# Performance work log

Hardware: AMD Instinct MI355X
Metric: run time of the kernel (lower is better)

## Reference

```python
import jax, jax.numpy as jnp
import numpy as np

HEADS = 8
DIM_HEAD = 64
SCALE = DIM_HEAD ** -0.5


def entmax15(z, axis=-1):
    """Exact 1.5-entmax via the sort-based algorithm (Peters & Martins 2019)."""
    z = z / 2.0
    z = z - jnp.max(z, axis=axis, keepdims=True)  # shift-invariant, for stability
    zs = -jnp.sort(-z, axis=axis)  # descending
    n = z.shape[axis]
    k = jnp.arange(1, n + 1, dtype=z.dtype)
    mean = jnp.cumsum(zs, axis=axis) / k
    mean_sq = jnp.cumsum(zs * zs, axis=axis) / k
    ss = k * (mean_sq - mean * mean)
    delta = (1.0 - ss) / k
    tau = mean - jnp.sqrt(jnp.maximum(delta, 0.0))
    support = (tau <= zs).astype(jnp.int32)
    k_star = jnp.sum(support, axis=axis, keepdims=True)  # support size >= 1
    tau_star = jnp.take_along_axis(tau, k_star - 1, axis=axis)
    return jnp.square(jnp.maximum(z - tau_star, 0.0))


def setup_inputs() -> dict:
    key = jax.random.key(0)
    k1, k2, k3 = jax.random.split(key, 3)
    b, n, dim = 4, 1024, 512
    inner = HEADS * DIM_HEAD  # 512
    x = jax.random.normal(k1, (b, n, dim), dtype=jnp.float32)
    w_qkv = jax.random.normal(k2, (dim, inner * 3), dtype=jnp.float32) * 0.02
    w_out = jax.random.normal(k3, (inner, dim), dtype=jnp.float32) * 0.02
    return {"x": x, "w_qkv": w_qkv, "w_out": w_out}


def reference(x, w_qkv, w_out):
    b, n, dim = x.shape
    h, d = HEADS, DIM_HEAD
    qkv = x @ w_qkv  # [b, n, 3*h*d]
    q, k, v = jnp.split(qkv, 3, axis=-1)
    # [b, n, h*d] -> [b, h, n, d]
    def to_heads(t):
        return t.reshape(b, n, h, d).transpose(0, 2, 1, 3)
    q, k, v = to_heads(q) * SCALE, to_heads(k), to_heads(v)
    sim = jnp.einsum('bhid,bhjd->bhij', q, k)  # [b, h, n, n]
    attn = entmax15(sim, axis=-1)
    out = jnp.einsum('bhij,bhjd->bhid', attn, v)  # [b, h, n, d]
    out = out.transpose(0, 2, 1, 3).reshape(b, n, h * d)
    return out @ w_out
```

## Files before the change

### kernel.cpp

```cpp
#include <hip/hip_runtime.h>
#include <stdint.h>
#include <stddef.h>


typedef __attribute__((ext_vector_type(4))) float f32x4;
typedef __attribute__((ext_vector_type(2))) float f32x2;
typedef __attribute__((ext_vector_type(8))) short bf16x8;
typedef __attribute__((ext_vector_type(4))) uint32_t u32x4;
typedef __attribute__((ext_vector_type(2))) uint32_t u32x2;

__device__ inline unsigned short f2bf(float f) {
    union { float f; uint32_t u; } cv; cv.f = f;
    uint32_t u = cv.u;
    return (unsigned short)((u + 0x7fffu + ((u >> 16) & 1u)) >> 16);
}
__device__ inline uint32_t packbf2(float lo, float hi) {
    uint32_t r;
    asm("v_cvt_pk_bf16_f32 %0, %1, %2" : "=v"(r) : "v"(lo), "v"(hi));
    return r;
}
__device__ inline void gl_lds16(const short* g, short* l) {
    __builtin_amdgcn_global_load_lds(
        (const __attribute__((address_space(1))) void*)g,
        (__attribute__((address_space(3))) void*)l, 16, 0, 0);
}
__device__ inline f32x2 vmax2(f32x2 a, f32x2 b) { return __builtin_elementwise_max(a, b); }
__device__ inline f32x2 vfma2(f32x2 a, f32x2 b, f32x2 c) { return __builtin_elementwise_fma(a, b, c); }

__global__ __launch_bounds__(256) void convert_all(const float* __restrict__ x,
                                                   const float* __restrict__ wqkv,
                                                   const float* __restrict__ wout,
                                                   short* __restrict__ xb,
                                                   short* __restrict__ wqkvt,
                                                   short* __restrict__ woutt) {
    __shared__ float tl[32][33];
    const int bid = blockIdx.x;
    const int t = threadIdx.x;
    if (bid < 1024) {
        int base = bid * 2048 + t * 8;
        f32x4 v0 = *(const f32x4*)(x + base);
        f32x4 v1 = *(const f32x4*)(x + base + 4);
        u32x4 o = {packbf2(v0[0], v0[1]), packbf2(v0[2], v0[3]),
                   packbf2(v1[0], v1[1]), packbf2(v1[2], v1[3])};
        *(u32x4*)(xb + base) = o;
        return;
    }
    const float* src; short* dst; int NC, tn, tk;
    if (bid < 1024 + 768) {
        int idx = bid - 1024; tn = idx % 48; tk = idx / 48; src = wqkv; dst = wqkvt; NC = 1536;
    } else {
        int idx = bid - 1792; tn = idx % 16; tk = idx / 16; src = wout; dst = woutt; NC = 512;
    }
    const int row = t >> 3, c4 = (t & 7) * 4;
    f32x4 v = *(const f32x4*)(src + (size_t)(tk * 32 + row) * NC + tn * 32 + c4);
    tl[row][c4 + 0] = v[0]; tl[row][c4 + 1] = v[1];
    tl[row][c4 + 2] = v[2]; tl[row][c4 + 3] = v[3];
    __syncthreads();
    float a = tl[c4 + 0][row], b = tl[c4 + 1][row];
    float c = tl[c4 + 2][row], d = tl[c4 + 3][row];
    u32x2 o = {packbf2(a, b), packbf2(c, d)};
    *(u32x2*)(dst + (size_t)(tn * 32 + row) * 512 + tk * 32 + c4) = o;
}

template<int NB, int MODE, int NT>
__global__ __launch_bounds__(256) void gemm_bf16(const short* __restrict__ A,
                                                 const short* __restrict__ Bt,
                                                 void* __restrict__ outp,
                                                 short* __restrict__ vt3,
                                                 short* __restrict__ kh) {
    constexpr int WN = NT / 2;
    constexpr int NFR = WN / 16;
    __shared__ __align__(16) short As[64 * 32];
    __shared__ __align__(16) short Bs[NT * 32];
    const int t = threadIdx.x;
    const int lane = t & 63;
    const int wv = t >> 6;
    const int quad = lane >> 4;
    const int l16 = lane & 15;
    const int bm = blockIdx.x / NB;
    const int bn = blockIdx.x % NB;
    const int wm = (wv & 1) * 32, wn = (wv >> 1) * WN;

    f32x4 acc[2][NFR];
    #pragma unroll
    for (int i = 0; i < 2; i++)
        #pragma unroll
        for (int j = 0; j < NFR; j++) acc[i][j] = (f32x4){0.f, 0.f, 0.f, 0.f};

    const int sr = t >> 2, sc = (t & 3) * 8;

    for (int kt = 0; kt < 16; kt++) {
        gl_lds16(A + (size_t)(bm * 64 + sr) * 512 + kt * 32 + sc, As + t * 8);
        #pragma unroll
        for (int i = 0; i < NT / 64; i++)
            gl_lds16(Bt + (size_t)(bn * NT + 64 * i + sr) * 512 + kt * 32 + sc,
                     Bs + 64 * i * 32 + t * 8);
        __syncthreads();
        bf16x8 af[2], bfr[NFR];
        #pragma unroll
        for (int mi = 0; mi < 2; mi++)
            af[mi] = *(const bf16x8*)(As + (wm + mi * 16 + l16) * 32 + quad * 8);
        #pragma unroll
        for (int ni = 0; ni < NFR; ni++)
            bfr[ni] = *(const bf16x8*)(Bs + (wn + ni * 16 + l16) * 32 + quad * 8);
        #pragma unroll
        for (int mi = 0; mi < 2; mi++)
            #pragma unroll
            for (int ni = 0; ni < NFR; ni++)
                acc[mi][ni] = __builtin_amdgcn_mfma_f32_16x16x32_bf16(af[mi], bfr[ni], acc[mi][ni], 0, 0, 0);
        __syncthreads();
    }

    if (MODE == 0) {
        if (bn < 4) {
            short* ob = (short*)outp;
            #pragma unroll
            for (int mi = 0; mi < 2; mi++)
                #pragma unroll
                for (int ni = 0; ni < NFR; ni++)
                    #pragma unroll
                    for (int rg = 0; rg < 4; rg++)
                        ob[(size_t)(bm * 64 + wm + mi * 16 + quad * 4 + rg) * 512
                           + bn * NT + wn + ni * 16 + l16] = (short)f2bf(acc[mi][ni][rg] * 0.0625f);
        } else if (bn < 8) {
            #pragma unroll
            for (int mi = 0; mi < 2; mi++) {
                int rowb = bm * 64 + wm + mi * 16 + quad * 4;
                int bbb = rowb >> 10, jj0 = rowb & 1023;
                #pragma unroll
                for (int ni = 0; ni < NFR; ni++) {
                    int c = bn * NT + wn + ni * 16 + l16 - 512;
                    int hh = c >> 6, dh = c & 63;
                    short* base = kh + (size_t)(bbb * 8 + hh) * 65536
                                  + (size_t)(jj0 >> 4) * 1024 + (dh >> 3) * 128 + (dh & 7);
                    #pragma unroll
                    for (int rg = 0; rg < 4; rg++)
                        base[((jj0 & 15) + rg) * 8] = (short)f2bf(acc[mi][ni][rg]);
                }
            }
        } else {
            #pragma unroll
            for (int mi = 0; mi < 2; mi++) {
                int rowb = bm * 64 + wm + mi * 16 + quad * 4;
                int bbb = rowb >> 10, j = rowb & 1023;
                #pragma unroll
                for (int ni = 0; ni < NFR; ni++) {
                    int vcol = bn * NT + wn + ni * 16 + l16 - 1024;
                    int hh = vcol >> 6, dd = vcol & 63;
                    u32x2 pk = {packbf2(acc[mi][ni][0], acc[mi][ni][1]),
                                packbf2(acc[mi][ni][2], acc[mi][ni][3])};
                    *(u32x2*)(vt3 + (size_t)(bbb * 8 + hh) * 65536
                              + (size_t)(j >> 3) * 512 + dd * 8 + (j & 7)) = pk;
                }
            }
        }
    } else {
        float* of = (float*)outp;
        #pragma unroll
        for (int mi = 0; mi < 2; mi++)
            #pragma unroll
            for (int ni = 0; ni < NFR; ni++)
                #pragma unroll
                for (int rg = 0; rg < 4; rg++)
                    of[(size_t)(bm * 64 + wm + mi * 16 + quad * 4 + rg) * 512
                       + bn * NT + wn + ni * 16 + l16] = acc[mi][ni][rg];
    }
}

__global__ __launch_bounds__(256, 4) void attn_entmax(const short* __restrict__ qb,
                                                      const short* __restrict__ kh,
                                                      const short* __restrict__ vt3,
                                                      short* __restrict__ oheads) {
    __shared__ __align__(16) unsigned char smem[32768];
    short* P_lds = (short*)smem;
    float* tbuf = (float*)smem;
    float* osum = (float*)smem;

    const int t = threadIdx.x;
    const int lane = t & 63;
    const int wv = t >> 6;
    const int quad = lane >> 4;
    const int l16 = lane & 15;

    const int xcd = blockIdx.x & 7;
    const int g = blockIdx.x >> 3;
    const int hb = xcd * 4 + (g >> 6);
    const int rt = g & 63;
    const int bb = hb >> 3, hh = hb & 7;
    const int r0 = rt * 16;

    bf16x8 a0, a1;
    {
        const short* qp = qb + (size_t)(bb * 1024 + r0 + l16) * 512 + hh * 64 + quad * 8;
        a0 = *(const bf16x8*)qp;
        a1 = *(const bf16x8*)(qp + 32);
    }

    const short* khh = kh + (size_t)(bb * 8 + hh) * 65536;
    const short* vb0 = vt3 + (size_t)(bb * 8 + hh) * 65536;

    f32x2 zT2[32];
    const int rown = quad * 4 + wv;
    for (int ci = 0; ci < 4; ci++) {
        f32x4 zc[4];
        #pragma unroll
        for (int f = 0; f < 4; f++) {
            int supl = f >> 1, jj = f & 1;
            int jtile = (ci * 2 + supl) * 8 + (wv + 4 * jj);
            const short* kp = khh + (size_t)jtile * 1024 + l16 * 8;
            bf16x8 b0 = *(const bf16x8*)(kp + quad * 128);
            bf16x8 b1 = *(const bf16x8*)(kp + (4 + quad) * 128);
            f32x4 acc = {0.f, 0.f, 0.f, 0.f};
            acc = __builtin_amdgcn_mfma_f32_16x16x32_bf16(a0, b0, acc, 0, 0, 0);
            acc = __builtin_amdgcn_mfma_f32_16x16x32_bf16(a1, b1, acc, 0, 0, 0);
            zc[f] = acc;
        }
        __syncthreads();
        #pragma unroll
        for (int f = 0; f < 4; f++) {
            int supl = f >> 1, jj = f & 1;
            int colc = supl * 128 + (wv + 4 * jj) * 16 + l16;
            #pragma unroll
            for (int rg = 0; rg < 4; rg++)
                tbuf[(quad * 4 + rg) * 268 + colc] = zc[f][rg];
        }
        __syncthreads();
        #pragma unroll
        for (int i = 0; i < 4; i++) {
            f32x4 v = *(const f32x4*)(tbuf + rown * 268 + i * 64 + l16 * 4);
            zT2[ci * 8 + i * 2 + 0] = (f32x2){v[0], v[1]};
            zT2[ci * 8 + i * 2 + 1] = (f32x2){v[2], v[3]};
        }
    }
    __syncthreads();

    float tau;
    {
        f32x2 m2 = zT2[0], p2 = zT2[0];
        f32x2 q2 = zT2[0] * zT2[0];
        #pragma unroll
        for (int i = 1; i < 32; i++) {
            f32x2 v = zT2[i];
            m2 = vmax2(m2, v);
            p2 = p2 + v;
            q2 = vfma2(v, v, q2);
        }
        float mx = fmaxf(m2[0], m2[1]);
        float s1 = p2[0] + p2[1];
        float s2 = q2[0] + q2[1];
        #pragma unroll
        for (int s = 1; s < 16; s <<= 1) {
            mx = fmaxf(mx, __shfl_xor(mx, s, 64));
            s1 += __shfl_xor(s1, s, 64);
            s2 += __shfl_xor(s2, s, 64);
        }
        float mean = s1 * (1.0f / 1024.0f);
        float disc = fmaxf(mean * mean - (s2 - 1.0f) * (1.0f / 1024.0f), 0.0f);
        tau = mean - __builtin_sqrtf(disc);
        tau = fminf(tau, mx - 0.03125f);
        tau = fmaxf(tau, mx - 1.0f);
    }

    const f32x2 zero2 = {0.f, 0.f};
    #pragma unroll 1
    for (int it = 0; it < 7; it++) {
        f32x2 tau2 = {tau, tau};
        f32x2 s1a = zero2, s1b = zero2, s2a = zero2, s2b = zero2;
        #pragma unroll
        for (int i = 0; i < 16; i++) {
            f32x2 ra = vmax2(zT2[i * 2] - tau2, zero2);
            f32x2 rb = vmax2(zT2[i * 2 + 1] - tau2, zero2);
            s1a = s1a + ra; s1b = s1b + rb;
            s2a = vfma2(ra, ra, s2a); s2b = vfma2(rb, rb, s2b);
        }
        float s1 = (s1a[0] + s1a[1]) + (s1b[0] + s1b[1]);
        float s2 = (s2a[0] + s2a[1]) + (s2b[0] + s2b[1]);
        #pragma unroll
        for (int s = 1; s < 16; s <<= 1) {
            s1 += __shfl_xor(s1, s, 64);
            s2 += __shfl_xor(s2, s, 64);
        }
        tau += (s2 - 1.0f) * 0.5f * __builtin_amdgcn_rcpf(s1);
    }

    {
        const f32x2 tau2 = {tau, tau};
        const int dg = l16;
        const int ra = rown & 7;
        #pragma unroll
        for (int ci = 0; ci < 4; ci++)
            #pragma unroll
            for (int i = 0; i < 4; i++) {
                f32x2 r01 = vmax2(zT2[ci * 8 + i * 2] - tau2, zero2);
                f32x2 r23 = vmax2(zT2[ci * 8 + i * 2 + 1] - tau2, zero2);
                f32x2 p01 = r01 * r01, p23 = r23 * r23;
                u32x2 pk = {packbf2(p01[0], p01[1]), packbf2(p23[0], p23[1])};
                int jb = ci * 32 + i * 8 + (dg >> 1);
                *(u32x2*)(P_lds + rown * 1024 + ((jb ^ ra) << 3) + (dg & 1) * 4) = pk;
            }
    }
    __syncthreads();

    f32x4 oacc[4];
    #pragma unroll
    for (int nt = 0; nt < 4; nt++) oacc[nt] = (f32x4){0.f, 0.f, 0.f, 0.f};
    const int lra = l16 & 7;
    #pragma unroll
    for (int sup = 0; sup < 8; sup++) {
        int jb = sup * 16 + wv * 4 + quad;
        bf16x8 pf = *(const bf16x8*)(P_lds + l16 * 1024 + ((jb ^ lra) << 3));
        const short* vs = vb0 + (size_t)jb * 512;
        #pragma unroll
        for (int nt = 0; nt < 4; nt++) {
            bf16x8 bv = *(const bf16x8*)(vs + (nt * 16 + l16) * 8);
            oacc[nt] = __builtin_amdgcn_mfma_f32_16x16x32_bf16(pf, bv, oacc[nt], 0, 0, 0);
        }
    }
    __syncthreads();

    #pragma unroll
    for (int nt = 0; nt < 4; nt++)
        #pragma unroll
        for (int rg = 0; rg < 4; rg++)
            osum[(wv * 16 + quad * 4 + rg) * 68 + nt * 16 + l16] = oacc[nt][rg];
    __syncthreads();
    #pragma unroll
    for (int i = 0; i < 2; i++) {
        int idx = t + 256 * i;
        int r = idx >> 5, dp = idx & 31;
        float e0 = 0.f, e1 = 0.f;
        #pragma unroll
        for (int w = 0; w < 4; w++) {
            e0 += osum[(w * 16 + r) * 68 + dp * 2];
            e1 += osum[(w * 16 + r) * 68 + dp * 2 + 1];
        }
        *(uint32_t*)(oheads + (size_t)(bb * 1024 + r0 + r) * 512 + hh * 64 + dp * 2) = packbf2(e0, e1);
    }
}

extern "C" void kernel_launch(void* const* d_in, const int* in_sizes, int n_in,
                              void* d_out, int out_size, void* d_ws, size_t ws_size,
                              hipStream_t stream) {
    (void)in_sizes; (void)n_in; (void)out_size; (void)ws_size;
    const float* x     = (const float*)d_in[0];
    const float* w_qkv = (const float*)d_in[1];
    const float* w_out = (const float*)d_in[2];
    float* out = (float*)d_out;

    char* ws = (char*)d_ws;
    short* qb    = (short*)(ws);
    short* kh    = (short*)(ws + 4194304);
    short* vt3   = (short*)(ws + 8388608);
    short* ohead = (short*)(ws + 12582912);
    short* xb    = (short*)(ws + 16777216);
    short* wqkvt = (short*)(ws + 20971520);
    short* woutt = (short*)(ws + 22544384);

    convert_all<<<dim3(2048), dim3(256), 0, stream>>>(x, w_qkv, w_out, xb, wqkvt, woutt);
    gemm_bf16<12, 0, 128><<<dim3(64 * 12), dim3(256), 0, stream>>>(xb, wqkvt, (void*)qb, vt3, kh);
    attn_entmax<<<dim3(2048), dim3(256), 0, stream>>>(qb, kh, vt3, ohead);
    gemm_bf16<8, 1, 64><<<dim3(64 * 8), dim3(256), 0, stream>>>(ohead, woutt, (void*)out, nullptr, nullptr);
}
```

Measured before the change: 126.5 us.

## Double-buffer GEMM LDS tiles and use DPP row reductions in entmax

```diff
diff --git a/kernel.cpp b/kernel.cpp
--- a/kernel.cpp
+++ b/kernel.cpp
@@ -26,6 +26,23 @@
 }
 __device__ inline f32x2 vmax2(f32x2 a, f32x2 b) { return __builtin_elementwise_max(a, b); }
 __device__ inline f32x2 vfma2(f32x2 a, f32x2 b, f32x2 c) { return __builtin_elementwise_fma(a, b, c); }
+
+template<int C> __device__ inline float rsum(float x) {
+    int v = __builtin_amdgcn_update_dpp(0, __builtin_bit_cast(int, x), C, 0xf, 0xf, true);
+    return x + __builtin_bit_cast(float, v);
+}
+template<int C> __device__ inline float rmax(float x) {
+    int v = __builtin_amdgcn_update_dpp(0, __builtin_bit_cast(int, x), C, 0xf, 0xf, true);
+    return fmaxf(x, __builtin_bit_cast(float, v));
+}
+__device__ inline float red16_sum(float x) {
+    x = rsum<0x128>(x); x = rsum<0x124>(x); x = rsum<0x122>(x); x = rsum<0x121>(x);
+    return x;
+}
+__device__ inline float red16_max(float x) {
+    x = rmax<0x128>(x); x = rmax<0x124>(x); x = rmax<0x122>(x); x = rmax<0x121>(x);
+    return x;
+}
 
 __global__ __launch_bounds__(256) void convert_all(const float* __restrict__ x,
                                                    const float* __restrict__ wqkv,
@@ -70,8 +87,8 @@
                                                  short* __restrict__ kh) {
     constexpr int WN = NT / 2;
     constexpr int NFR = WN / 16;
-    __shared__ __align__(16) short As[64 * 32];
-    __shared__ __align__(16) short Bs[NT * 32];
+    __shared__ __align__(16) short As[2][64 * 32];
+    __shared__ __align__(16) short Bs[2][NT * 32];
     const int t = threadIdx.x;
     const int lane = t & 63;
     const int wv = t >> 6;
@@ -88,21 +105,31 @@
         for (int j = 0; j < NFR; j++) acc[i][j] = (f32x4){0.f, 0.f, 0.f, 0.f};
 
     const int sr = t >> 2, sc = (t & 3) * 8;
+    const short* Abase = A + (size_t)(bm * 64 + sr) * 512 + sc;
+    const short* Bbase = Bt + (size_t)(bn * NT + sr) * 512 + sc;
+
+    gl_lds16(Abase, &As[0][t * 8]);
+    #pragma unroll
+    for (int i = 0; i < NT / 64; i++)
+        gl_lds16(Bbase + (size_t)(64 * i) * 512, &Bs[0][64 * i * 32 + t * 8]);
+    __syncthreads();
 
     for (int kt = 0; kt < 16; kt++) {
-        gl_lds16(A + (size_t)(bm * 64 + sr) * 512 + kt * 32 + sc, As + t * 8);
-        #pragma unroll
-        for (int i = 0; i < NT / 64; i++)
-            gl_lds16(Bt + (size_t)(bn * NT + 64 * i + sr) * 512 + kt * 32 + sc,
-                     Bs + 64 * i * 32 + t * 8);
-        __syncthreads();
+        const int cur = kt & 1;
+        if (kt < 15) {
+            gl_lds16(Abase + (kt + 1) * 32, &As[cur ^ 1][t * 8]);
+            #pragma unroll
+            for (int i = 0; i < NT / 64; i++)
+                gl_lds16(Bbase + (size_t)(64 * i) * 512 + (kt + 1) * 32,
+                         &Bs[cur ^ 1][64 * i * 32 + t * 8]);
+        }
         bf16x8 af[2], bfr[NFR];
         #pragma unroll
         for (int mi = 0; mi < 2; mi++)
-            af[mi] = *(const bf16x8*)(As + (wm + mi * 16 + l16) * 32 + quad * 8);
+            af[mi] = *(const bf16x8*)(&As[cur][(wm + mi * 16 + l16) * 32 + quad * 8]);
         #pragma unroll
         for (int ni = 0; ni < NFR; ni++)
-            bfr[ni] = *(const bf16x8*)(Bs + (wn + ni * 16 + l16) * 32 + quad * 8);
+            bfr[ni] = *(const bf16x8*)(&Bs[cur][(wn + ni * 16 + l16) * 32 + quad * 8]);
         #pragma unroll
         for (int mi = 0; mi < 2; mi++)
             #pragma unroll
@@ -245,15 +272,9 @@
             p2 = p2 + v;
             q2 = vfma2(v, v, q2);
         }
-        float mx = fmaxf(m2[0], m2[1]);
-        float s1 = p2[0] + p2[1];
-        float s2 = q2[0] + q2[1];
-        #pragma unroll
-        for (int s = 1; s < 16; s <<= 1) {
-            mx = fmaxf(mx, __shfl_xor(mx, s, 64));
-            s1 += __shfl_xor(s1, s, 64);
-            s2 += __shfl_xor(s2, s, 64);
-        }
+        float mx = red16_max(fmaxf(m2[0], m2[1]));
+        float s1 = red16_sum(p2[0] + p2[1]);
+        float s2 = red16_sum(q2[0] + q2[1]);
         float mean = s1 * (1.0f / 1024.0f);
         float disc = fmaxf(mean * mean - (s2 - 1.0f) * (1.0f / 1024.0f), 0.0f);
         tau = mean - __builtin_sqrtf(disc);
@@ -273,13 +294,8 @@
             s1a = s1a + ra; s1b = s1b + rb;
             s2a = vfma2(ra, ra, s2a); s2b = vfma2(rb, rb, s2b);
         }
-        float s1 = (s1a[0] + s1a[1]) + (s1b[0] + s1b[1]);
-        float s2 = (s2a[0] + s2a[1]) + (s2b[0] + s2b[1]);
-        #pragma unroll
-        for (int s = 1; s < 16; s <<= 1) {
-            s1 += __shfl_xor(s1, s, 64);
-            s2 += __shfl_xor(s2, s, 64);
-        }
+        float s1 = red16_sum((s1a[0] + s1a[1]) + (s1b[0] + s1b[1]));
+        float s2 = red16_sum((s2a[0] + s2a[1]) + (s2b[0] + s2b[1]));
         tau += (s2 - 1.0f) * 0.5f * __builtin_amdgcn_rcpf(s1);
     }
 
```

After: 128.8 us. Within noise of the previous version (+1.8%).
